# Kernel tuning notes

Measured on AMD Instinct MI355X. Metric: run time of the kernel, lower is better.

Reference implementation:

```python
import jax, jax.numpy as jnp
import numpy as np

B, N, F_IN, F_OUT = 8, 2048, 128, 64
ALPHA = 0.2  # LeakyReLU negative slope
NEG_BIG = -9e15


def setup_inputs() -> dict:
    key = jax.random.key(0)
    k1, k2, k3, k4 = jax.random.split(key, 4)
    x = jax.random.normal(k1, (B, N, F_IN), dtype=jnp.float32)
    adj = jax.random.randint(k2, (B, N, N), 0, 2, dtype=jnp.int32)
    # xavier-uniform-ish init scale for faithfulness (gain=1.414)
    w_lim = 1.414 * np.sqrt(6.0 / (F_IN + F_OUT))
    a_lim = 1.414 * np.sqrt(6.0 / (2 * F_OUT + 1))
    weight = jax.random.uniform(k3, (F_IN, F_OUT), minval=-w_lim, maxval=w_lim, dtype=jnp.float32)
    weight2 = jax.random.uniform(k4, (2 * F_OUT, 1), minval=-a_lim, maxval=a_lim, dtype=jnp.float32)
    return {"x": x, "adj": adj, "weight": weight, "weight2": weight2}


def reference(x, adj, weight, weight2):
    # Linear projection: [B, N, F_out]
    wh = jnp.einsum("bnf,fo->bno", x, weight)
    # Additive GAT decomposition of concat-score:
    # e_ij = leakyrelu(a1 . Wh_i + a2 . Wh_j)  == original concat @ weight2
    a1 = weight2[:F_OUT, 0]   # [F_out]
    a2 = weight2[F_OUT:, 0]   # [F_out]
    s1 = wh @ a1              # [B, N]
    s2 = wh @ a2              # [B, N]
    e = s1[:, :, None] + s2[:, None, :]          # [B, N, N]
    e = jnp.where(e > 0, e, ALPHA * e)            # LeakyReLU
    e = jnp.where(adj > 0, e, NEG_BIG)            # mask non-edges
    attention = jax.nn.softmax(e, axis=2)         # [B, N, N]
    # dropout is identity in eval mode (training=False)
    out = jnp.einsum("bij,bjo->bio", attention, wh)  # [B, N, F_out]
    return jax.nn.elu(out)
```

## Files before the change

kernel.cpp:

```cpp
#include <hip/hip_runtime.h>
#include <cstdint>
#include <cstddef>

#define B_    8
#define N_    2048
#define FIN   128
#define FOUT  64
#define ALPHA 0.2f
#define NEG_BIG -9.0e15f

typedef __attribute__((ext_vector_type(8))) _Float16 half8;
typedef __attribute__((ext_vector_type(4))) float float4v;

__global__ __launch_bounds__(256, 4) void k1_wh(
    const float* __restrict__ x, const float* __restrict__ W,
    const float* __restrict__ w2, _Float16* __restrict__ whT,
    float* __restrict__ s1, float* __restrict__ s2)
{
    int t = threadIdx.x, lane = t & 63, w = t >> 6;
    float a1 = w2[lane], a2 = w2[FOUT + lane];
    int rowBase = blockIdx.x * 32 + w * 8;
    for (int rr = 0; rr < 8; ++rr) {
        int row = __builtin_amdgcn_readfirstlane(rowBase + rr);
        const float* xr = x + (size_t)row * FIN;
        float acc = 0.f;
        #pragma unroll
        for (int k = 0; k < FIN; ++k)
            acc = fmaf(xr[k], W[k * FOUT + lane], acc);
        int b = row >> 11, j = row & (N_ - 1);
        whT[((size_t)b * FOUT + lane) * N_ + j] = (_Float16)acc;
        float p1 = acc * a1, p2 = acc * a2;
        #pragma unroll
        for (int m = 32; m >= 1; m >>= 1) {
            p1 += __shfl_xor(p1, m);
            p2 += __shfl_xor(p2, m);
        }
        if (lane == 0) { s1[row] = p1; s2[row] = p2; }
    }
}

__global__ __launch_bounds__(256, 4) void k2_attn(
    const int* __restrict__ adj, const _Float16* __restrict__ whT,
    const float* __restrict__ s1, const float* __restrict__ s2,
    float* __restrict__ out)
{
    __shared__ __attribute__((aligned(16))) _Float16 pT[16][520];
    __shared__ float lL[16];
    __shared__ float smaxL[4];

    int t = threadIdx.x, lane = t & 63, w = t >> 6;
    int b = blockIdx.x >> 7;
    int i0 = (blockIdx.x & 127) << 4;

    const float4* s2v = (const float4*)(s2 + (size_t)b * N_);
    float4 ua = s2v[t], ub = s2v[t + 256];
    float vm = fmaxf(fmaxf(fmaxf(ua.x, ua.y), fmaxf(ua.z, ua.w)),
                     fmaxf(fmaxf(ub.x, ub.y), fmaxf(ub.z, ub.w)));
    #pragma unroll
    for (int m = 32; m >= 1; m >>= 1) vm = fmaxf(vm, __shfl_xor(vm, m));
    if (lane == 0) smaxL[w] = vm;
    __syncthreads();
    float s2max = fmaxf(fmaxf(smaxL[0], smaxL[1]), fmaxf(smaxL[2], smaxL[3]));

    int l15 = lane & 15, quad = lane >> 4;
    int f0 = w * 16;

    float s1r[4], negmh[4], lacc[4];
    #pragma unroll
    for (int rr = 0; rr < 4; ++rr) {
        float sv = s1[(size_t)b * N_ + i0 + w * 4 + rr];
        float mh = sv + s2max;
        mh = fmaxf(mh, ALPHA * mh);
        s1r[rr] = sv;
        negmh[rr] = -mh;
        lacc[rr] = 0.f;
    }

    float4v acc = {0, 0, 0, 0};
    const _Float16* wB = whT + ((size_t)b * FOUT + f0 + l15) * N_ + quad * 8;

    for (int jc = 0; jc < N_; jc += 512) {
        const float* s2c = s2 + (size_t)b * N_ + jc + lane * 8;
        float4 sa = *(const float4*)s2c;
        float4 sb = *(const float4*)(s2c + 4);
        float ss[8] = {sa.x, sa.y, sa.z, sa.w, sb.x, sb.y, sb.z, sb.w};

        #pragma unroll
        for (int rr = 0; rr < 4; ++rr) {
            int r = w * 4 + rr;
            const int* ap = adj + ((size_t)b * N_ + i0 + r) * N_ + jc + lane * 8;
            int4 aj0 = *(const int4*)ap;
            int4 aj1 = *(const int4*)(ap + 4);
            int aa[8] = {aj0.x, aj0.y, aj0.z, aj0.w, aj1.x, aj1.y, aj1.z, aj1.w};
            half8 pf;
            float ls = 0.f;
            #pragma unroll
            for (int e = 0; e < 8; ++e) {
                float v = s1r[rr] + ss[e];
                v = fmaxf(v, ALPHA * v);
                v = (aa[e] > 0) ? v : NEG_BIG;
                float tt = fmaxf(v + negmh[rr], -76.f);
                float p = __expf(tt);
                ls += p;
                pf[e] = (_Float16)p;
            }
            lacc[rr] += ls;
            *(half8*)&pT[r][lane * 8] = pf;
        }

        if (jc == N_ - 512) {
            #pragma unroll
            for (int rr = 0; rr < 4; ++rr) {
                float v = lacc[rr];
                #pragma unroll
                for (int m = 32; m >= 1; m >>= 1) v += __shfl_xor(v, m);
                if (lane == 0) lL[w * 4 + rr] = v;
            }
        }
        __syncthreads();

        const _Float16* wp = wB + jc;
        #pragma unroll
        for (int kk = 0; kk < 16; ++kk) {
            half8 af = *(const half8*)&pT[l15][kk * 32 + quad * 8];
            half8 bf = *(const half8*)(wp + kk * 32);
            acc = __builtin_amdgcn_mfma_f32_16x16x32_f16(af, bf, acc, 0, 0, 0);
        }
        __syncthreads();
    }

    #pragma unroll
    for (int reg = 0; reg < 4; ++reg) {
        int row = quad * 4 + reg;
        float val = acc[reg] / lL[row];
        val = (val > 0.f) ? val : (__expf(val) - 1.f);
        out[((size_t)b * N_ + i0 + row) * FOUT + f0 + l15] = val;
    }
}

extern "C" void kernel_launch(void* const* d_in, const int* in_sizes, int n_in,
                              void* d_out, int out_size, void* d_ws, size_t ws_size,
                              hipStream_t stream) {
    const float* x   = (const float*)d_in[0];
    const int*   adj = (const int*)d_in[1];
    const float* W   = (const float*)d_in[2];
    const float* w2  = (const float*)d_in[3];
    float* out = (float*)d_out;

    _Float16* whT = (_Float16*)d_ws;
    float* s1 = (float*)((char*)d_ws + (size_t)B_ * FOUT * N_ * 2);
    float* s2 = s1 + (size_t)B_ * N_;

    k1_wh<<<(B_ * N_) / 32, 256, 0, stream>>>(x, W, w2, whT, s1, s2);
    k2_attn<<<(B_ * N_) / 16, 256, 0, stream>>>(adj, whT, s1, s2, out);
}
```

Measured before the change: 255.6 us.

## Use split-fp16 MFMA for projection and exp2-based masked softmax scores

The projection kernel moves from per-lane scalar FMA loops to MFMA. Inputs and weights are split into fp16 hi/lo pairs so the products keep near-fp32 accuracy, and a small pre-kernel transposes and converts W. The attention kernel folds LeakyReLU and the row max into two precomputed log2-scaled affine terms, uses a native exp2, and masks the probability to zero instead of substituting a huge negative. This cuts ALU work in both the projection and the score computation, at the cost of an extra kernel launch and three MFMAs per chunk.

Result: faster. 219.7 us (-14.0%).

```diff
diff --git a/kernel.cpp b/kernel.cpp
--- a/kernel.cpp
+++ b/kernel.cpp
@@ -7,35 +7,109 @@
 #define FIN   128
 #define FOUT  64
 #define ALPHA 0.2f
-#define NEG_BIG -9.0e15f
+#define LOG2E 1.4426950408889634f
 
 typedef __attribute__((ext_vector_type(8))) _Float16 half8;
+typedef __attribute__((ext_vector_type(4))) _Float16 half4;
 typedef __attribute__((ext_vector_type(4))) float float4v;
 
-__global__ __launch_bounds__(256, 4) void k1_wh(
-    const float* __restrict__ x, const float* __restrict__ W,
+__global__ __launch_bounds__(256) void k0_convW(
+    const float* __restrict__ W, _Float16* __restrict__ WtG)
+{
+    int o = blockIdx.x * 256 + threadIdx.x;
+    int f = o >> 7, k = o & 127;
+    float v = W[k * FOUT + f];
+    _Float16 hi = (_Float16)v;
+    _Float16 lo = (_Float16)(v - (float)hi);
+    WtG[o] = hi;
+    WtG[FOUT * FIN + o] = lo;
+}
+
+__global__ __launch_bounds__(256, 2) void k1_wh(
+    const float* __restrict__ x, const _Float16* __restrict__ WtG,
     const float* __restrict__ w2, _Float16* __restrict__ whT,
     float* __restrict__ s1, float* __restrict__ s2)
 {
+    __shared__ __attribute__((aligned(16))) _Float16 xth[32][136];
+    __shared__ __attribute__((aligned(16))) _Float16 xtl[32][136];
+    __shared__ float s1p[4][32];
+    __shared__ float s2p[4][32];
+
     int t = threadIdx.x, lane = t & 63, w = t >> 6;
-    float a1 = w2[lane], a2 = w2[FOUT + lane];
-    int rowBase = blockIdx.x * 32 + w * 8;
-    for (int rr = 0; rr < 8; ++rr) {
-        int row = __builtin_amdgcn_readfirstlane(rowBase + rr);
-        const float* xr = x + (size_t)row * FIN;
-        float acc = 0.f;
-        #pragma unroll
-        for (int k = 0; k < FIN; ++k)
-            acc = fmaf(xr[k], W[k * FOUT + lane], acc);
-        int b = row >> 11, j = row & (N_ - 1);
-        whT[((size_t)b * FOUT + lane) * N_ + j] = (_Float16)acc;
-        float p1 = acc * a1, p2 = acc * a2;
-        #pragma unroll
-        for (int m = 32; m >= 1; m >>= 1) {
-            p1 += __shfl_xor(p1, m);
-            p2 += __shfl_xor(p2, m);
-        }
-        if (lane == 0) { s1[row] = p1; s2[row] = p2; }
+    int b = blockIdx.x >> 6;
+    int r0 = (blockIdx.x & 63) << 5;
+    const float* xb = x + ((size_t)b * N_ + r0) * FIN;
+
+    #pragma unroll
+    for (int j = 0; j < 4; ++j) {
+        int idx = t + j * 256;
+        int row = idx >> 5;
+        int k0 = (idx & 31) * 4;
+        float4 v = ((const float4*)xb)[idx];
+        float vv[4] = {v.x, v.y, v.z, v.w};
+        half4 h, l;
+        #pragma unroll
+        for (int e = 0; e < 4; ++e) {
+            _Float16 hi = (_Float16)vv[e];
+            h[e] = hi;
+            l[e] = (_Float16)(vv[e] - (float)hi);
+        }
+        *(half4*)&xth[row][k0] = h;
+        *(half4*)&xtl[row][k0] = l;
+    }
+    __syncthreads();
+
+    int l15 = lane & 15, quad = lane >> 4;
+    int f0 = w * 16;
+
+    half8 bh[4], bl[4];
+    const _Float16* wgh = WtG + (f0 + l15) * FIN + quad * 8;
+    #pragma unroll
+    for (int c = 0; c < 4; ++c) {
+        bh[c] = *(const half8*)(wgh + c * 32);
+        bl[c] = *(const half8*)(wgh + FOUT * FIN + c * 32);
+    }
+    float a1f = w2[f0 + l15], a2f = w2[FOUT + f0 + l15];
+
+    #pragma unroll
+    for (int rt = 0; rt < 2; ++rt) {
+        float4v acc = {0.f, 0.f, 0.f, 0.f};
+        #pragma unroll
+        for (int c = 0; c < 4; ++c) {
+            half8 ah = *(const half8*)&xth[rt * 16 + l15][c * 32 + quad * 8];
+            half8 al = *(const half8*)&xtl[rt * 16 + l15][c * 32 + quad * 8];
+            acc = __builtin_amdgcn_mfma_f32_16x16x32_f16(ah, bh[c], acc, 0, 0, 0);
+            acc = __builtin_amdgcn_mfma_f32_16x16x32_f16(ah, bl[c], acc, 0, 0, 0);
+            acc = __builtin_amdgcn_mfma_f32_16x16x32_f16(al, bh[c], acc, 0, 0, 0);
+        }
+        half4 hv;
+        #pragma unroll
+        for (int reg = 0; reg < 4; ++reg) hv[reg] = (_Float16)acc[reg];
+        *(half4*)(whT + ((size_t)b * FOUT + f0 + l15) * N_ + r0 + rt * 16 + quad * 4) = hv;
+
+        #pragma unroll
+        for (int reg = 0; reg < 4; ++reg) {
+            float v1 = acc[reg] * a1f;
+            float v2 = acc[reg] * a2f;
+            #pragma unroll
+            for (int m = 1; m <= 8; m <<= 1) {
+                v1 += __shfl_xor(v1, m);
+                v2 += __shfl_xor(v2, m);
+            }
+            if (l15 == 0) {
+                s1p[w][rt * 16 + quad * 4 + reg] = v1;
+                s2p[w][rt * 16 + quad * 4 + reg] = v2;
+            }
+        }
+    }
+    __syncthreads();
+    if (t < 32) {
+        float v = s1p[0][t] + s1p[1][t] + s1p[2][t] + s1p[3][t];
+        s1[(size_t)b * N_ + r0 + t] = v;
+    } else if (t < 64) {
+        int r = t - 32;
+        float v = s2p[0][r] + s2p[1][r] + s2p[2][r] + s2p[3][r];
+        s2[(size_t)b * N_ + r0 + r] = v;
     }
 }
 
@@ -53,9 +127,9 @@
     int i0 = (blockIdx.x & 127) << 4;
 
     const float4* s2v = (const float4*)(s2 + (size_t)b * N_);
-    float4 ua = s2v[t], ub = s2v[t + 256];
-    float vm = fmaxf(fmaxf(fmaxf(ua.x, ua.y), fmaxf(ua.z, ua.w)),
-                     fmaxf(fmaxf(ub.x, ub.y), fmaxf(ub.z, ub.w)));
+    float4 ua_ = s2v[t], ub_ = s2v[t + 256];
+    float vm = fmaxf(fmaxf(fmaxf(ua_.x, ua_.y), fmaxf(ua_.z, ua_.w)),
+                     fmaxf(fmaxf(ub_.x, ub_.y), fmaxf(ub_.z, ub_.w)));
     #pragma unroll
     for (int m = 32; m >= 1; m >>= 1) vm = fmaxf(vm, __shfl_xor(vm, m));
     if (lane == 0) smaxL[w] = vm;
@@ -65,18 +139,18 @@
     int l15 = lane & 15, quad = lane >> 4;
     int f0 = w * 16;
 
-    float s1r[4], negmh[4], lacc[4];
+    float c1[4], c2[4], lacc[4];
     #pragma unroll
     for (int rr = 0; rr < 4; ++rr) {
         float sv = s1[(size_t)b * N_ + i0 + w * 4 + rr];
-        float mh = sv + s2max;
-        mh = fmaxf(mh, ALPHA * mh);
-        s1r[rr] = sv;
-        negmh[rr] = -mh;
+        float mm = sv + s2max;
+        float mh = fmaxf(mm, ALPHA * mm);
+        c1[rr] = (sv - mh) * LOG2E;
+        c2[rr] = (ALPHA * sv - mh) * LOG2E;
         lacc[rr] = 0.f;
     }
 
-    float4v acc = {0, 0, 0, 0};
+    float4v acc = {0.f, 0.f, 0.f, 0.f};
     const _Float16* wB = whT + ((size_t)b * FOUT + f0 + l15) * N_ + quad * 8;
 
     for (int jc = 0; jc < N_; jc += 512) {
@@ -84,6 +158,12 @@
         float4 sa = *(const float4*)s2c;
         float4 sb = *(const float4*)(s2c + 4);
         float ss[8] = {sa.x, sa.y, sa.z, sa.w, sb.x, sb.y, sb.z, sb.w};
+        float u[8], ual[8];
+        #pragma unroll
+        for (int e = 0; e < 8; ++e) {
+            u[e] = ss[e] * LOG2E;
+            ual[e] = u[e] * ALPHA;
+        }
 
         #pragma unroll
         for (int rr = 0; rr < 4; ++rr) {
@@ -96,11 +176,13 @@
             float ls = 0.f;
             #pragma unroll
             for (int e = 0; e < 8; ++e) {
-                float v = s1r[rr] + ss[e];
-                v = fmaxf(v, ALPHA * v);
-                v = (aa[e] > 0) ? v : NEG_BIG;
-                float tt = fmaxf(v + negmh[rr], -76.f);
-                float p = __expf(tt);
+                float t2 = fmaxf(c1[rr] + u[e], c2[rr] + ual[e]);
+#if __has_builtin(__builtin_amdgcn_exp2f)
+                float p = __builtin_amdgcn_exp2f(t2);
+#else
+                float p = exp2f(t2);
+#endif
+                p = (aa[e] > 0) ? p : 0.f;
                 ls += p;
                 pf[e] = (_Float16)p;
             }
@@ -150,7 +232,9 @@
     _Float16* whT = (_Float16*)d_ws;
     float* s1 = (float*)((char*)d_ws + (size_t)B_ * FOUT * N_ * 2);
     float* s2 = s1 + (size_t)B_ * N_;
-
-    k1_wh<<<(B_ * N_) / 32, 256, 0, stream>>>(x, W, w2, whT, s1, s2);
+    _Float16* WtG = (_Float16*)(s2 + (size_t)B_ * N_);
+
+    k0_convW<<<32, 256, 0, stream>>>(W, WtG);
+    k1_wh<<<(B_ * N_) / 32, 256, 0, stream>>>(x, WtG, w2, whT, s1, s2);
     k2_attn<<<(B_ * N_) / 16, 256, 0, stream>>>(adj, whT, s1, s2, out);
 }
```
